# Optimization experiments

Measured on AMD Instinct MI355X. Metric: run time of the kernel, lower is better.

Reference implementation:

```python
import jax, jax.numpy as jnp
import numpy as np

N_NODES = 100000
N_EDGES = 1600000
F_IN = 128
HID = 128
N_LAYERS = 4
N_CLASSES = 10
N_GRAPHS = 512
BN_EPS = 1e-5


def setup_inputs() -> dict:
    key = jax.random.key(0)
    ks = jax.random.split(key, 16)
    x = jax.random.normal(ks[0], (N_NODES, F_IN), dtype=jnp.float32)
    edge_index = jax.random.randint(ks[1], (2, N_EDGES), 0, N_NODES, dtype=jnp.int64)
    edge_attr = jax.random.normal(ks[2], (N_EDGES, 8), dtype=jnp.float32)
    batch = jnp.sort(jax.random.randint(ks[3], (N_NODES,), 0, N_GRAPHS, dtype=jnp.int64))
    # Per-layer MLP params (in-dim is 128 for all layers since F_IN == HID).
    s1 = 1.0 / np.sqrt(F_IN)
    s2 = 1.0 / np.sqrt(2 * HID)
    W1 = jax.random.uniform(ks[4], (N_LAYERS, F_IN, 2 * HID), minval=-s1, maxval=s1, dtype=jnp.float32)
    b1 = jax.random.uniform(ks[5], (N_LAYERS, 2 * HID), minval=-s1, maxval=s1, dtype=jnp.float32)
    gamma1 = jnp.ones((N_LAYERS, 2 * HID), dtype=jnp.float32)
    beta1 = jnp.zeros((N_LAYERS, 2 * HID), dtype=jnp.float32)
    W2 = jax.random.uniform(ks[6], (N_LAYERS, 2 * HID, HID), minval=-s2, maxval=s2, dtype=jnp.float32)
    b2 = jax.random.uniform(ks[7], (N_LAYERS, HID), minval=-s2, maxval=s2, dtype=jnp.float32)
    sf = 1.0 / np.sqrt(HID * N_LAYERS)
    fcW = jax.random.uniform(ks[8], (HID * N_LAYERS, N_CLASSES), minval=-sf, maxval=sf, dtype=jnp.float32)
    fcb = jax.random.uniform(ks[9], (N_CLASSES,), minval=-sf, maxval=sf, dtype=jnp.float32)
    return {"x": x, "edge_index": edge_index, "edge_attr": edge_attr, "batch": batch,
            "W1": W1, "b1": b1, "gamma1": gamma1, "beta1": beta1,
            "W2": W2, "b2": b2, "fcW": fcW, "fcb": fcb}


def reference(x, edge_index, edge_attr, batch, W1, b1, gamma1, beta1, W2, b2, fcW, fcb):
    # edge_attr is unused by the original forward.
    src, dst = edge_index[0], edge_index[1]
    n = x.shape[0]
    # In-degree for mean aggregation (messages flow src -> dst in PyG).
    deg = jax.ops.segment_sum(jnp.ones((src.shape[0],), x.dtype), dst, num_segments=n)
    inv_deg = 1.0 / jnp.maximum(deg, 1.0)
    h = x
    xs = []
    for i in range(N_LAYERS):
        # GINConv, eps=0, aggr='mean': nn(x + mean_j h_j)
        agg = jax.ops.segment_sum(h[src], dst, num_segments=n) * inv_deg[:, None]
        z = h + agg
        z = z @ W1[i] + b1[i]                      # [N, 2H]
        mu = jnp.mean(z, axis=0)
        var = jnp.mean(jnp.square(z - mu), axis=0)  # biased var (BN training mode)
        z = gamma1[i] * (z - mu) * jax.lax.rsqrt(var + BN_EPS) + beta1[i]
        z = jax.nn.relu(z)
        z = z @ W2[i] + b2[i]                      # [N, H]
        h = jax.nn.relu(z)
        xs.append(h)
    xcat = jnp.concatenate(xs, axis=1)             # [N, H*L]
    # global_mean_pool over graph ids
    gsum = jax.ops.segment_sum(xcat, batch, num_segments=N_GRAPHS)
    gcnt = jax.ops.segment_sum(jnp.ones((n,), xcat.dtype), batch, num_segments=N_GRAPHS)
    pooled = gsum / jnp.maximum(gcnt, 1.0)[:, None]
    logits = pooled @ fcW + fcb
    return jax.nn.log_softmax(logits, axis=-1)
```

## Files before the change

kernel.cpp:

```cpp
#include <hip/hip_runtime.h>
#include <cstdint>
#include <cstddef>

#define NN 100000
#define NE 1600000
#define FD 128
#define HD2 256
#define NLAYERS 4
#define NGR 512
#define NCLS 10
#define BNEPS 1e-5f
#define G1TILES 1563
#define GEMM_GRID 521
#define MLP_GRID 256
#define EB 6250
#define NB 391
#define NSLICE 8
#define SLICEW 12500

typedef unsigned short ushort_t;
typedef short bf16x8 __attribute__((ext_vector_type(8)));
typedef float f32x4 __attribute__((ext_vector_type(4)));

__device__ __forceinline__ float bfl(unsigned short u) {
  unsigned v = ((unsigned)u) << 16;
  return __builtin_bit_cast(float, v);
}
__device__ __forceinline__ unsigned short fbf(float f) {
  unsigned u = __builtin_bit_cast(unsigned, f);
  unsigned r = (u + 0x7FFFu + ((u >> 16) & 1u)) >> 16;
  return (unsigned short)r;
}

__global__ void k_init_detect(const int* ei, int* flag, int* degi) {
  int i = blockIdx.x * 256 + threadIdx.x;
  if (i < NN) degi[i] = 0;
  if (blockIdx.x == 0) {
    __shared__ int nz;
    if (threadIdx.x == 0) nz = 0;
    __syncthreads();
    if (ei[2 * threadIdx.x + 1] != 0) atomicAdd(&nz, 1);
    __syncthreads();
    if (threadIdx.x == 0) flag[0] = (nz == 0) ? 1 : 0;
  }
}

__global__ void k_repack(const int* ei, const int* batch, const int* flag,
                         int* src32, int* dst32, int* batch32) {
  int i = blockIdx.x * 256 + threadIdx.x;
  const bool wide = (flag[0] != 0);
  if (i < NE) {
    src32[i] = wide ? ei[2 * i] : ei[i];
    dst32[i] = wide ? ei[2 * (NE + i)] : ei[NE + i];
  }
  if (i < NN) batch32[i] = wide ? batch[2 * i] : batch[i];
}

__global__ void k_deg8(const int* __restrict__ dst, int* degi) {
  int slice = blockIdx.x & (NSLICE - 1);
  int e = (blockIdx.x >> 3) * 256 + threadIdx.x;
  if (e >= NE) return;
  int d = dst[e];
  int lo = slice * SLICEW;
  if (d >= lo && d < lo + SLICEW) atomicAdd(&degi[d], 1);
}

__global__ void k_scan1(const int* degi, int* rowptr, int* bsum) {
  __shared__ int s[256];
  int t = threadIdx.x;
  int i = blockIdx.x * 256 + t;
  int v = (i < NN) ? degi[i] : 0;
  s[t] = v;
  __syncthreads();
  for (int off = 1; off < 256; off <<= 1) {
    int x = (t >= off) ? s[t - off] : 0;
    __syncthreads();
    s[t] += x;
    __syncthreads();
  }
  if (i < NN) rowptr[i] = s[t] - v;
  if (t == 255) bsum[blockIdx.x] = s[255];
}

__global__ void k_scan2_gstats(int* bsum, int nb, const int* __restrict__ batch,
                               int* __restrict__ gstart, int* __restrict__ gcnti) {
  __shared__ int s[512];
  int t = threadIdx.x;
  int v = (t < nb) ? bsum[t] : 0;
  s[t] = v;
  __syncthreads();
  for (int off = 1; off < 512; off <<= 1) {
    int x = (t >= off) ? s[t - off] : 0;
    __syncthreads();
    s[t] += x;
    __syncthreads();
  }
  if (t < nb) bsum[t] = s[t] - v;
  if (t < NGR) {
    int g = t;
    int lo = 0, hi = NN;
    while (lo < hi) { int m = (lo + hi) >> 1; if (batch[m] < g) lo = m + 1; else hi = m; }
    int st = lo;
    hi = NN;
    while (lo < hi) { int m = (lo + hi) >> 1; if (batch[m] < g + 1) lo = m + 1; else hi = m; }
    gstart[g] = st;
    gcnti[g] = lo - st;
  }
}

__global__ void k_scan3_cursor(int* rowptr, const int* bsum, int* cursor,
                               const int* degi, float* inv_deg) {
  int i = blockIdx.x * 256 + threadIdx.x;
  if (i < NN) {
    int r = rowptr[i] + bsum[blockIdx.x];
    rowptr[i] = r;
    cursor[i] = r;
    inv_deg[i] = 1.f / fmaxf((float)degi[i], 1.f);
  }
  if (i == 0) rowptr[NN] = NE;
}

__global__ void k_scatter8(const int* __restrict__ src, const int* __restrict__ dst,
                           int* cursor, int* csr) {
  int slice = blockIdx.x & (NSLICE - 1);
  int e = (blockIdx.x >> 3) * 256 + threadIdx.x;
  if (e >= NE) return;
  int d = dst[e];
  int lo = slice * SLICEW;
  if (d >= lo && d < lo + SLICEW) {
    int p = atomicAdd(&cursor[d], 1);
    csr[p] = src[e];
  }
}

__global__ void k_cvt_x(const float* __restrict__ x, ushort_t* __restrict__ xb) {
  int i = blockIdx.x * 256 + threadIdx.x;
  if (i >= NN * FD / 8) return;
  const float4* p = (const float4*)x + (size_t)i * 2;
  float4 a = p[0], b = p[1];
  bf16x8 o;
  o[0] = (short)fbf(a.x); o[1] = (short)fbf(a.y);
  o[2] = (short)fbf(a.z); o[3] = (short)fbf(a.w);
  o[4] = (short)fbf(b.x); o[5] = (short)fbf(b.y);
  o[6] = (short)fbf(b.z); o[7] = (short)fbf(b.w);
  *(bf16x8*)&xb[(size_t)i * 8] = o;
}

__global__ void k_cvt_w(const float* __restrict__ W1, const float* __restrict__ W2,
                        ushort_t* __restrict__ W1t, ushort_t* __restrict__ W2t) {
  int idx = blockIdx.x * 256 + threadIdx.x;
  if (idx >= NLAYERS * FD * HD2) return;
  int l = idx >> 15, r = idx & 32767;
  {
    int n = r >> 7, k = r & 127;
    W1t[(size_t)l * 32768 + n * 128 + k] = fbf(W1[(size_t)l * 32768 + k * 256 + n]);
  }
  {
    int n = r >> 8, k = r & 255;
    W2t[(size_t)l * 32768 + n * 256 + k] = fbf(W2[(size_t)l * 32768 + k * 128 + n]);
  }
}

__global__ void k_agg(const ushort_t* __restrict__ h, const int* __restrict__ rowptr,
                      const int* __restrict__ csr, const float* __restrict__ inv_deg,
                      ushort_t* __restrict__ tout, float* bnsum) {
  if (blockIdx.x == 0) {
    bnsum[threadIdx.x] = 0.f;
    bnsum[HD2 + threadIdx.x] = 0.f;
  }
  const int wave = threadIdx.x >> 6;
  const int lane = threadIdx.x & 63;
  const int q = lane >> 4, sub = lane & 15;
  const int node = blockIdx.x * 16 + wave * 4 + q;
  const uint4* h16 = (const uint4*)h;
  int beg = rowptr[node];
  int deg = rowptr[node + 1] - beg;
  int m1 = max(deg, __shfl_xor(deg, 16));
  int maxd = max(m1, __shfl_xor(m1, 32));
  float a0 = 0.f, a1 = 0.f, a2 = 0.f, a3 = 0.f;
  float a4 = 0.f, a5 = 0.f, a6 = 0.f, a7 = 0.f;
  int j = 0;
  for (; j + 8 <= maxd; j += 8) {
    uint4 p[8];
#pragma unroll
    for (int u = 0; u < 8; ++u) {
      bool valid = (j + u) < deg;
      int idx = beg + (valid ? j + u : 0);
      int s = csr[idx];
      uint4 v = h16[(size_t)s * 16 + sub];
      p[u].x = valid ? v.x : 0u;
      p[u].y = valid ? v.y : 0u;
      p[u].z = valid ? v.z : 0u;
      p[u].w = valid ? v.w : 0u;
    }
#pragma unroll
    for (int u = 0; u < 8; ++u) {
      a0 += bfl((unsigned short)(p[u].x & 0xFFFF));
      a1 += bfl((unsigned short)(p[u].x >> 16));
      a2 += bfl((unsigned short)(p[u].y & 0xFFFF));
      a3 += bfl((unsigned short)(p[u].y >> 16));
      a4 += bfl((unsigned short)(p[u].z & 0xFFFF));
      a5 += bfl((unsigned short)(p[u].z >> 16));
      a6 += bfl((unsigned short)(p[u].w & 0xFFFF));
      a7 += bfl((unsigned short)(p[u].w >> 16));
    }
  }
  for (; j < maxd; ++j) {
    bool valid = j < deg;
    int idx = beg + (valid ? j : 0);
    int s = csr[idx];
    uint4 v = h16[(size_t)s * 16 + sub];
    if (valid) {
      a0 += bfl((unsigned short)(v.x & 0xFFFF));
      a1 += bfl((unsigned short)(v.x >> 16));
      a2 += bfl((unsigned short)(v.y & 0xFFFF));
      a3 += bfl((unsigned short)(v.y >> 16));
      a4 += bfl((unsigned short)(v.z & 0xFFFF));
      a5 += bfl((unsigned short)(v.z >> 16));
      a6 += bfl((unsigned short)(v.w & 0xFFFF));
      a7 += bfl((unsigned short)(v.w >> 16));
    }
  }
  float id = inv_deg[node];
  uint4 c = h16[(size_t)node * 16 + sub];
  float o0 = bfl((unsigned short)(c.x & 0xFFFF)) + a0 * id;
  float o1 = bfl((unsigned short)(c.x >> 16)) + a1 * id;
  float o2 = bfl((unsigned short)(c.y & 0xFFFF)) + a2 * id;
  float o3 = bfl((unsigned short)(c.y >> 16)) + a3 * id;
  float o4 = bfl((unsigned short)(c.z & 0xFFFF)) + a4 * id;
  float o5 = bfl((unsigned short)(c.z >> 16)) + a5 * id;
  float o6 = bfl((unsigned short)(c.w & 0xFFFF)) + a6 * id;
  float o7 = bfl((unsigned short)(c.w >> 16)) + a7 * id;
  uint4 ow;
  ow.x = (unsigned)fbf(o0) | ((unsigned)fbf(o1) << 16);
  ow.y = (unsigned)fbf(o2) | ((unsigned)fbf(o3) << 16);
  ow.z = (unsigned)fbf(o4) | ((unsigned)fbf(o5) << 16);
  ow.w = (unsigned)fbf(o6) | ((unsigned)fbf(o7) << 16);
  ((uint4*)tout)[(size_t)node * 16 + sub] = ow;
}

__launch_bounds__(256, 2)
__global__ void k_zstat(const ushort_t* __restrict__ A, const ushort_t* __restrict__ Bt,
                        const float* __restrict__ bias, float* __restrict__ bnsum) {
  __shared__ ushort_t Bs[256 * 128];
  __shared__ ushort_t As[64 * 128];
  const int tid = threadIdx.x;
#pragma unroll
  for (int i = 0; i < 16; ++i) {
    int chunk = tid + 256 * i;
    int n = chunk >> 4, c = chunk & 15;
    bf16x8 v = *(const bf16x8*)&Bt[n * 128 + c * 8];
    *(bf16x8*)((char*)Bs + n * 256 + ((c * 16) ^ ((n & 7) << 4))) = v;
  }
  const int wv = tid >> 6, ln = tid & 63;
  const int lr = ln & 15, lg = ln >> 4;
  float bb[16];
#pragma unroll
  for (int nt = 0; nt < 16; ++nt) bb[nt] = bias[nt * 16 + lr];
  float s0[16] = {}, s1[16] = {};

  for (int t = blockIdx.x; t < G1TILES; t += GEMM_GRID) {
    int row0 = t * 64;
#pragma unroll
    for (int i = 0; i < 4; ++i) {
      int chunk = tid + 256 * i;
      int r = chunk >> 4, c = chunk & 15;
      int grow = row0 + r; if (grow >= NN) grow = NN - 1;
      bf16x8 v = *(const bf16x8*)&A[(size_t)grow * FD + c * 8];
      *(bf16x8*)((char*)As + r * 256 + ((c * 16) ^ ((r & 7) << 4))) = v;
    }
    __syncthreads();
    int arow = wv * 16 + lr;
    bf16x8 af[4];
#pragma unroll
    for (int ks = 0; ks < 4; ++ks)
      af[ks] = *(bf16x8*)((char*)As + arow * 256 + ((ks * 64 + lg * 16) ^ ((arow & 7) << 4)));
    f32x4 acc[16];
#pragma unroll
    for (int nt = 0; nt < 16; ++nt) acc[nt] = (f32x4){0.f, 0.f, 0.f, 0.f};
#pragma unroll
    for (int nt = 0; nt < 16; ++nt) {
      int bn = nt * 16 + lr;
#pragma unroll
      for (int ks = 0; ks < 4; ++ks) {
        bf16x8 bfr = *(bf16x8*)((char*)Bs + bn * 256 + ((ks * 64 + lg * 16) ^ ((bn & 7) << 4)));
        acc[nt] = __builtin_amdgcn_mfma_f32_16x16x32_bf16(af[ks], bfr, acc[nt], 0, 0, 0);
      }
    }
    __syncthreads();
#pragma unroll
    for (int nt = 0; nt < 16; ++nt) {
#pragma unroll
      for (int j = 0; j < 4; ++j) {
        int grow = row0 + wv * 16 + lg * 4 + j;
        if (grow < NN) {
          float zf = acc[nt][j] + bb[nt];
          s0[nt] += zf;
          s1[nt] += zf * zf;
        }
      }
    }
  }
  __syncthreads();
  float* ls = (float*)As;
  ls[tid] = 0.f; ls[tid + 256] = 0.f;
  __syncthreads();
#pragma unroll
  for (int nt = 0; nt < 16; ++nt) {
    int col = nt * 16 + lr;
    atomicAdd(&ls[col], s0[nt]);
    atomicAdd(&ls[col + 256], s1[nt]);
  }
  __syncthreads();
  if (tid < 256) {
    atomicAdd(&bnsum[tid], ls[tid]);
    atomicAdd(&bnsum[HD2 + tid], ls[tid + 256]);
  }
}

__launch_bounds__(512, 2)
__global__ void k_mlp(const ushort_t* __restrict__ T, const ushort_t* __restrict__ W1t,
                      const ushort_t* __restrict__ W2t, const float* __restrict__ b1,
                      const float* __restrict__ b2, const float* __restrict__ bnsum,
                      const float* __restrict__ gamma, const float* __restrict__ beta,
                      ushort_t* __restrict__ Hout) {
  __shared__ ushort_t W1s[256 * 128];
  __shared__ ushort_t W2s[128 * 256];
  __shared__ ushort_t ZR[64 * 256];
  const int tid = threadIdx.x;
#pragma unroll
  for (int i = 0; i < 8; ++i) {
    int chunk = tid + 512 * i;
    int n = chunk >> 4, c = chunk & 15;
    bf16x8 v = *(const bf16x8*)&W1t[n * 128 + c * 8];
    *(bf16x8*)((char*)W1s + n * 256 + ((c * 16) ^ ((n & 7) << 4))) = v;
  }
#pragma unroll
  for (int i = 0; i < 8; ++i) {
    int chunk = tid + 512 * i;
    int n = chunk >> 5, c = chunk & 31;
    bf16x8 v = *(const bf16x8*)&W2t[n * 256 + c * 8];
    *(bf16x8*)((char*)W2s + n * 512 + ((c * 16) ^ ((n & 7) << 4))) = v;
  }
  const int wv = tid >> 6, ln = tid & 63;
  const int lr = ln & 15, lg = ln >> 4;
  const int mrow = (wv & 3) * 16;
  const int nh = wv >> 2;
  float a1v[8], a2v[8], bb1[8];
#pragma unroll
  for (int nt = 0; nt < 8; ++nt) {
    int c = (nh * 8 + nt) * 16 + lr;
    float mu = bnsum[c] * (1.f / (float)NN);
    float var = fmaxf(bnsum[HD2 + c] * (1.f / (float)NN) - mu * mu, 0.f);
    float g = gamma[c] * rsqrtf(var + BNEPS);
    a1v[nt] = g;
    a2v[nt] = beta[c] - mu * g;
    bb1[nt] = b1[c];
  }
  float bb2[4];
#pragma unroll
  for (int nt2 = 0; nt2 < 4; ++nt2) bb2[nt2] = b2[nh * 64 + nt2 * 16 + lr];
  __syncthreads();

  for (int t = blockIdx.x; t < G1TILES; t += MLP_GRID) {
    int row0 = t * 64;
    int grow = row0 + mrow + lr; if (grow >= NN) grow = NN - 1;
    bf16x8 af[4];
#pragma unroll
    for (int ks = 0; ks < 4; ++ks)
      af[ks] = *(const bf16x8*)&T[(size_t)grow * FD + ks * 32 + lg * 8];
    f32x4 acc1[8];
#pragma unroll
    for (int nt = 0; nt < 8; ++nt) acc1[nt] = (f32x4){0.f, 0.f, 0.f, 0.f};
#pragma unroll
    for (int nt = 0; nt < 8; ++nt) {
      int bn = (nh * 8 + nt) * 16 + lr;
#pragma unroll
      for (int ks = 0; ks < 4; ++ks) {
        bf16x8 bfr = *(bf16x8*)((char*)W1s + bn * 256 + ((ks * 64 + lg * 16) ^ ((bn & 7) << 4)));
        acc1[nt] = __builtin_amdgcn_mfma_f32_16x16x32_bf16(af[ks], bfr, acc1[nt], 0, 0, 0);
      }
    }
#pragma unroll
    for (int nt = 0; nt < 8; ++nt) {
      int col = (nh * 8 + nt) * 16 + lr;
#pragma unroll
      for (int j = 0; j < 4; ++j) {
        int row = mrow + lg * 4 + j;
        float z = acc1[nt][j] + bb1[nt];
        float f = fmaxf(z * a1v[nt] + a2v[nt], 0.f);
        int byte = row * 512 + ((((col >> 3) << 4) ^ ((row & 7) << 4))) + (col & 7) * 2;
        *(ushort_t*)((char*)ZR + byte) = fbf(f);
      }
    }
    __syncthreads();
    int zrow = mrow + lr;
    bf16x8 af2[8];
#pragma unroll
    for (int ks2 = 0; ks2 < 8; ++ks2) {
      int c2 = ks2 * 4 + lg;
      af2[ks2] = *(bf16x8*)((char*)ZR + zrow * 512 + ((c2 * 16) ^ ((zrow & 7) << 4)));
    }
    __syncthreads();
    f32x4 acc2[4];
#pragma unroll
    for (int nt2 = 0; nt2 < 4; ++nt2) acc2[nt2] = (f32x4){0.f, 0.f, 0.f, 0.f};
#pragma unroll
    for (int nt2 = 0; nt2 < 4; ++nt2) {
      int bn2 = nh * 64 + nt2 * 16 + lr;
#pragma unroll
      for (int ks2 = 0; ks2 < 8; ++ks2) {
        int c2 = ks2 * 4 + lg;
        bf16x8 bfr2 = *(bf16x8*)((char*)W2s + bn2 * 512 + ((c2 * 16) ^ ((bn2 & 7) << 4)));
        acc2[nt2] = __builtin_amdgcn_mfma_f32_16x16x32_bf16(af2[ks2], bfr2, acc2[nt2], 0, 0, 0);
      }
    }
#pragma unroll
    for (int nt2 = 0; nt2 < 4; ++nt2) {
      int col = nh * 64 + nt2 * 16 + lr;
#pragma unroll
      for (int j = 0; j < 4; ++j) {
        int hrow = row0 + mrow + lg * 4 + j;
        if (hrow < NN) Hout[(size_t)hrow * FD + col] = fbf(fmaxf(acc2[nt2][j] + bb2[nt2], 0.f));
      }
    }
  }
}

__launch_bounds__(256)
__global__ void k_pool_fc(const ushort_t* __restrict__ hb, const int* __restrict__ gstart,
                          const int* __restrict__ gcnti, const float* __restrict__ fcW,
                          const float* __restrict__ fcb, float* __restrict__ out) {
  __shared__ float pool4[4][512];
  __shared__ float wred[4][NCLS];
  int g = blockIdx.x, t = threadIdx.x;
  int start = gstart[g], cnt = gcnti[g];
  int chunk = t & 63, ro = t >> 6;
  int L = chunk >> 4, cc = (chunk & 15) * 8;
  const ushort_t* hL = hb + (size_t)L * NN * FD;
  float s[8] = {};
  for (int r = start + ro; r < start + cnt; r += 4) {
    bf16x8 v = *(const bf16x8*)&hL[(size_t)r * FD + cc];
#pragma unroll
    for (int j = 0; j < 8; ++j) s[j] += bfl((unsigned short)v[j]);
  }
#pragma unroll
  for (int j = 0; j < 8; ++j) pool4[ro][chunk * 8 + j] = s[j];
  __syncthreads();
  float inv = 1.f / fmaxf((float)cnt, 1.f);
  float pA = (pool4[0][t] + pool4[1][t] + pool4[2][t] + pool4[3][t]) * inv;
  float pB = (pool4[0][t + 256] + pool4[1][t + 256] + pool4[2][t + 256] + pool4[3][t + 256]) * inv;
  float pacc[NCLS];
#pragma unroll
  for (int c = 0; c < NCLS; ++c)
    pacc[c] = pA * fcW[t * NCLS + c] + pB * fcW[(t + 256) * NCLS + c];
#pragma unroll
  for (int off = 32; off > 0; off >>= 1)
#pragma unroll
    for (int c = 0; c < NCLS; ++c) pacc[c] += __shfl_down(pacc[c], off);
  if ((t & 63) == 0)
#pragma unroll
    for (int c = 0; c < NCLS; ++c) wred[t >> 6][c] = pacc[c];
  __syncthreads();
  if (t == 0) {
    float lg[NCLS];
    float mx = -1e30f;
#pragma unroll
    for (int c = 0; c < NCLS; ++c) {
      lg[c] = wred[0][c] + wred[1][c] + wred[2][c] + wred[3][c] + fcb[c];
      mx = fmaxf(mx, lg[c]);
    }
    float se = 0.f;
#pragma unroll
    for (int c = 0; c < NCLS; ++c) se += expf(lg[c] - mx);
    float lse = mx + logf(se);
#pragma unroll
    for (int c = 0; c < NCLS; ++c) out[(size_t)g * NCLS + c] = lg[c] - lse;
  }
}

extern "C" void kernel_launch(void* const* d_in, const int* in_sizes, int n_in,
                              void* d_out, int out_size, void* d_ws, size_t ws_size,
                              hipStream_t stream) {
  const float* x      = (const float*)d_in[0];
  const int*   ei     = (const int*)d_in[1];
  const int*   batch  = (const int*)d_in[3];
  const float* W1     = (const float*)d_in[4];
  const float* b1     = (const float*)d_in[5];
  const float* gamma1 = (const float*)d_in[6];
  const float* beta1  = (const float*)d_in[7];
  const float* W2     = (const float*)d_in[8];
  const float* b2     = (const float*)d_in[9];
  const float* fcW    = (const float*)d_in[10];
  const float* fcb    = (const float*)d_in[11];
  float* out = (float*)d_out;

  char* p = (char*)d_ws;
  auto alloc = [&](size_t bytes) {
    char* r = p;
    p += (bytes + 255) & ~(size_t)255;
    return r;
  };
  ushort_t* xbf   = (ushort_t*)alloc((size_t)NN * FD * 2);
  ushort_t* tbuf  = (ushort_t*)alloc((size_t)NN * FD * 2);
  ushort_t* hb    = (ushort_t*)alloc((size_t)NLAYERS * NN * FD * 2);
  ushort_t* W1t   = (ushort_t*)alloc((size_t)NLAYERS * FD * HD2 * 2);
  ushort_t* W2t   = (ushort_t*)alloc((size_t)NLAYERS * FD * HD2 * 2);
  float* inv_deg  = (float*)alloc((size_t)NN * 4);
  float* bnsum    = (float*)alloc(2 * HD2 * 4);
  int* degi       = (int*)alloc((size_t)NN * 4);
  int* rowptr     = (int*)alloc((size_t)(NN + 1) * 4);
  int* cursor     = (int*)alloc((size_t)NN * 4);
  int* csr        = (int*)alloc((size_t)NE * 4);
  int* bsum       = (int*)alloc(512 * 4);
  int* src32      = (int*)alloc((size_t)NE * 4);
  int* dst32      = (int*)alloc((size_t)NE * 4);
  int* batch32    = (int*)alloc((size_t)NN * 4);
  int* gcnti      = (int*)alloc((size_t)NGR * 4);
  int* gstart     = (int*)alloc((size_t)NGR * 4);
  int* flag       = (int*)alloc(256);

  k_init_detect<<<NB, 256, 0, stream>>>(ei, flag, degi);
  k_repack<<<EB, 256, 0, stream>>>(ei, batch, flag, src32, dst32, batch32);
  k_deg8<<<EB * NSLICE, 256, 0, stream>>>(dst32, degi);
  k_scan1<<<NB, 256, 0, stream>>>(degi, rowptr, bsum);
  k_scan2_gstats<<<1, 512, 0, stream>>>(bsum, NB, batch32, gstart, gcnti);
  k_scan3_cursor<<<NB, 256, 0, stream>>>(rowptr, bsum, cursor, degi, inv_deg);
  k_scatter8<<<EB * NSLICE, 256, 0, stream>>>(src32, dst32, cursor, csr);
  k_cvt_x<<<(NN * FD / 8 + 255) / 256, 256, 0, stream>>>(x, xbf);
  k_cvt_w<<<(NLAYERS * FD * HD2 + 255) / 256, 256, 0, stream>>>(W1, W2, W1t, W2t);

  const ushort_t* hin = xbf;
  for (int L = 0; L < NLAYERS; ++L) {
    k_agg<<<NN / 16, 256, 0, stream>>>(hin, rowptr, csr, inv_deg, tbuf, bnsum);
    k_zstat<<<GEMM_GRID, 256, 0, stream>>>(tbuf, W1t + (size_t)L * FD * HD2,
                                           b1 + (size_t)L * HD2, bnsum);
    k_mlp<<<MLP_GRID, 512, 0, stream>>>(tbuf, W1t + (size_t)L * FD * HD2,
                                        W2t + (size_t)L * FD * HD2,
                                        b1 + (size_t)L * HD2, b2 + (size_t)L * FD,
                                        bnsum, gamma1 + (size_t)L * HD2,
                                        beta1 + (size_t)L * HD2,
                                        hb + (size_t)L * NN * FD);
    hin = hb + (size_t)L * NN * FD;
  }
  k_pool_fc<<<NGR, 256, 0, stream>>>(hb, gstart, gcnti, fcW, fcb, out);
}
```

Baseline: 794.8 us.

## Compute batchnorm statistics from input Gram matrix instead of full first GEMM

Measured after the change: 851.9 us. +7.2%, slower.

```diff
diff --git a/kernel.cpp b/kernel.cpp
--- a/kernel.cpp
+++ b/kernel.cpp
@@ -11,8 +11,8 @@
 #define NCLS 10
 #define BNEPS 1e-5f
 #define G1TILES 1563
-#define GEMM_GRID 521
 #define MLP_GRID 256
+#define GRAM_GRID 256
 #define EB 6250
 #define NB 391
 #define NSLICE 8
@@ -163,11 +163,8 @@
 
 __global__ void k_agg(const ushort_t* __restrict__ h, const int* __restrict__ rowptr,
                       const int* __restrict__ csr, const float* __restrict__ inv_deg,
-                      ushort_t* __restrict__ tout, float* bnsum) {
-  if (blockIdx.x == 0) {
-    bnsum[threadIdx.x] = 0.f;
-    bnsum[HD2 + threadIdx.x] = 0.f;
-  }
+                      ushort_t* __restrict__ tout, float* sbuf) {
+  if (blockIdx.x == 0 && threadIdx.x < FD) sbuf[threadIdx.x] = 0.f;
   const int wave = threadIdx.x >> 6;
   const int lane = threadIdx.x & 63;
   const int q = lane >> 4, sub = lane & 15;
@@ -239,82 +236,135 @@
   ((uint4*)tout)[(size_t)node * 16 + sub] = ow;
 }
 
-__launch_bounds__(256, 2)
-__global__ void k_zstat(const ushort_t* __restrict__ A, const ushort_t* __restrict__ Bt,
-                        const float* __restrict__ bias, float* __restrict__ bnsum) {
-  __shared__ ushort_t Bs[256 * 128];
-  __shared__ ushort_t As[64 * 128];
+__launch_bounds__(256)
+__global__ void k_gram(const ushort_t* __restrict__ T, float* __restrict__ Pg,
+                       float* __restrict__ sbuf) {
+  __shared__ ushort_t Tt[128 * 64];
   const int tid = threadIdx.x;
-#pragma unroll
-  for (int i = 0; i < 16; ++i) {
-    int chunk = tid + 256 * i;
-    int n = chunk >> 4, c = chunk & 15;
-    bf16x8 v = *(const bf16x8*)&Bt[n * 128 + c * 8];
-    *(bf16x8*)((char*)Bs + n * 256 + ((c * 16) ^ ((n & 7) << 4))) = v;
-  }
   const int wv = tid >> 6, ln = tid & 63;
   const int lr = ln & 15, lg = ln >> 4;
-  float bb[16];
-#pragma unroll
-  for (int nt = 0; nt < 16; ++nt) bb[nt] = bias[nt * 16 + lr];
-  float s0[16] = {}, s1[16] = {};
-
-  for (int t = blockIdx.x; t < G1TILES; t += GEMM_GRID) {
+  const int mbase = (wv >> 1) * 64, nbase = (wv & 1) * 64;
+  const int cst = tid & 15;
+  float sloc[8] = {};
+  f32x4 acc[4][4];
+#pragma unroll
+  for (int a = 0; a < 4; ++a)
+#pragma unroll
+    for (int b = 0; b < 4; ++b) acc[a][b] = (f32x4){0.f, 0.f, 0.f, 0.f};
+
+  for (int t = blockIdx.x; t < G1TILES; t += GRAM_GRID) {
     int row0 = t * 64;
 #pragma unroll
     for (int i = 0; i < 4; ++i) {
       int chunk = tid + 256 * i;
-      int r = chunk >> 4, c = chunk & 15;
-      int grow = row0 + r; if (grow >= NN) grow = NN - 1;
-      bf16x8 v = *(const bf16x8*)&A[(size_t)grow * FD + c * 8];
-      *(bf16x8*)((char*)As + r * 256 + ((c * 16) ^ ((r & 7) << 4))) = v;
-    }
-    __syncthreads();
-    int arow = wv * 16 + lr;
-    bf16x8 af[4];
-#pragma unroll
-    for (int ks = 0; ks < 4; ++ks)
-      af[ks] = *(bf16x8*)((char*)As + arow * 256 + ((ks * 64 + lg * 16) ^ ((arow & 7) << 4)));
-    f32x4 acc[16];
-#pragma unroll
-    for (int nt = 0; nt < 16; ++nt) acc[nt] = (f32x4){0.f, 0.f, 0.f, 0.f};
-#pragma unroll
-    for (int nt = 0; nt < 16; ++nt) {
-      int bn = nt * 16 + lr;
-#pragma unroll
-      for (int ks = 0; ks < 4; ++ks) {
-        bf16x8 bfr = *(bf16x8*)((char*)Bs + bn * 256 + ((ks * 64 + lg * 16) ^ ((bn & 7) << 4)));
-        acc[nt] = __builtin_amdgcn_mfma_f32_16x16x32_bf16(af[ks], bfr, acc[nt], 0, 0, 0);
-      }
-    }
-    __syncthreads();
-#pragma unroll
-    for (int nt = 0; nt < 16; ++nt) {
+      int r = chunk >> 4;
+      int grow = row0 + r;
+      uint4 v = (grow < NN) ? ((const uint4*)T)[(size_t)grow * 16 + cst]
+                            : make_uint4(0u, 0u, 0u, 0u);
+      unsigned short us[8];
+      us[0] = (unsigned short)(v.x & 0xFFFF); us[1] = (unsigned short)(v.x >> 16);
+      us[2] = (unsigned short)(v.y & 0xFFFF); us[3] = (unsigned short)(v.y >> 16);
+      us[4] = (unsigned short)(v.z & 0xFFFF); us[5] = (unsigned short)(v.z >> 16);
+      us[6] = (unsigned short)(v.w & 0xFFFF); us[7] = (unsigned short)(v.w >> 16);
+#pragma unroll
+      for (int jj = 0; jj < 8; ++jj) {
+        int j = (jj + (tid & 7)) & 7;
+        int f = cst * 8 + j;
+        int byte = f * 128 + ((((r >> 3) << 4) ^ ((f & 7) << 4))) + (r & 7) * 2;
+        *(ushort_t*)((char*)Tt + byte) = us[j];
+      }
+#pragma unroll
+      for (int j = 0; j < 8; ++j) sloc[j] += bfl(us[j]);
+    }
+    __syncthreads();
+#pragma unroll
+    for (int ks = 0; ks < 2; ++ks) {
+      bf16x8 bfr[4];
+#pragma unroll
+      for (int b = 0; b < 4; ++b) {
+        int fB = nbase + b * 16 + lr;
+        bfr[b] = *(bf16x8*)((char*)Tt + fB * 128 + ((((ks * 4 + lg) << 4) ^ ((fB & 7) << 4))));
+      }
+#pragma unroll
+      for (int a = 0; a < 4; ++a) {
+        int fA = mbase + a * 16 + lr;
+        bf16x8 afr = *(bf16x8*)((char*)Tt + fA * 128 + ((((ks * 4 + lg) << 4) ^ ((fA & 7) << 4))));
+#pragma unroll
+        for (int b = 0; b < 4; ++b)
+          acc[a][b] = __builtin_amdgcn_mfma_f32_16x16x32_bf16(afr, bfr[b], acc[a][b], 0, 0, 0);
+      }
+    }
+    __syncthreads();
+  }
+  float* sred = (float*)Tt;
+#pragma unroll
+  for (int j = 0; j < 8; ++j) sred[(tid >> 4) * 128 + cst * 8 + j] = sloc[j];
+  __syncthreads();
+  if (tid < FD) {
+    float v = 0.f;
+#pragma unroll
+    for (int g = 0; g < 16; ++g) v += sred[g * 128 + tid];
+    atomicAdd(&sbuf[tid], v);
+  }
+  float* P = Pg + (size_t)blockIdx.x * (FD * FD);
+#pragma unroll
+  for (int a = 0; a < 4; ++a)
+#pragma unroll
+    for (int b = 0; b < 4; ++b)
 #pragma unroll
       for (int j = 0; j < 4; ++j) {
-        int grow = row0 + wv * 16 + lg * 4 + j;
-        if (grow < NN) {
-          float zf = acc[nt][j] + bb[nt];
-          s0[nt] += zf;
-          s1[nt] += zf * zf;
-        }
-      }
-    }
-  }
-  __syncthreads();
-  float* ls = (float*)As;
-  ls[tid] = 0.f; ls[tid + 256] = 0.f;
-  __syncthreads();
-#pragma unroll
-  for (int nt = 0; nt < 16; ++nt) {
-    int col = nt * 16 + lr;
-    atomicAdd(&ls[col], s0[nt]);
-    atomicAdd(&ls[col + 256], s1[nt]);
-  }
-  __syncthreads();
-  if (tid < 256) {
-    atomicAdd(&bnsum[tid], ls[tid]);
-    atomicAdd(&bnsum[HD2 + tid], ls[tid + 256]);
+        int fm = mbase + a * 16 + (ln >> 4) * 4 + j;
+        int fn = nbase + b * 16 + lr;
+        P[fm * FD + fn] = acc[a][b][j];
+      }
+}
+
+__global__ void k_gred(const float* __restrict__ Pg, float* __restrict__ G) {
+  int idx = blockIdx.x * 256 + threadIdx.x;
+  float v = 0.f;
+  for (int b = 0; b < GRAM_GRID; ++b) v += Pg[(size_t)b * (FD * FD) + idx];
+  G[idx] = v;
+}
+
+__launch_bounds__(256)
+__global__ void k_bnfin2(const float* __restrict__ G, const float* __restrict__ sbuf,
+                         const float* __restrict__ W1, const float* __restrict__ b1,
+                         float* __restrict__ bnsum) {
+  __shared__ float Gs[FD * FD];
+  __shared__ float ws1[FD * 32];
+  const int tid = threadIdx.x;
+  for (int i = tid; i < FD * FD; i += 256) Gs[i] = G[i];
+  for (int i = tid; i < FD * 32; i += 256) {
+    int k = i >> 5, cl = i & 31;
+    ws1[i] = bfl(fbf(W1[k * HD2 + blockIdx.x * 32 + cl]));
+  }
+  __syncthreads();
+  const int cl = tid & 31, kg = tid >> 5;
+  float q = 0.f, sd = 0.f;
+  for (int k = kg * 16; k < kg * 16 + 16; ++k) {
+    float wk = ws1[k * 32 + cl];
+    float dot = 0.f;
+#pragma unroll 8
+    for (int k2 = 0; k2 < FD; ++k2) dot += Gs[k * FD + k2] * ws1[k2 * 32 + cl];
+    q += wk * dot;
+    sd += sbuf[k] * wk;
+  }
+  __syncthreads();
+  float* red = Gs;
+  red[tid] = q;
+  red[256 + tid] = sd;
+  __syncthreads();
+  if (tid < 32) {
+    float Q = 0.f, SD = 0.f;
+#pragma unroll
+    for (int g = 0; g < 8; ++g) {
+      Q += red[tid + 32 * g];
+      SD += red[256 + tid + 32 * g];
+    }
+    int c = blockIdx.x * 32 + tid;
+    float bb = b1[c];
+    bnsum[c] = SD + (float)NN * bb;
+    bnsum[HD2 + c] = Q + 2.f * bb * SD + (float)NN * bb * bb;
   }
 }
 
@@ -508,6 +558,9 @@
   ushort_t* W2t   = (ushort_t*)alloc((size_t)NLAYERS * FD * HD2 * 2);
   float* inv_deg  = (float*)alloc((size_t)NN * 4);
   float* bnsum    = (float*)alloc(2 * HD2 * 4);
+  float* Pg       = (float*)alloc((size_t)GRAM_GRID * FD * FD * 4);
+  float* Gm       = (float*)alloc((size_t)FD * FD * 4);
+  float* sbuf     = (float*)alloc((size_t)FD * 4);
   int* degi       = (int*)alloc((size_t)NN * 4);
   int* rowptr     = (int*)alloc((size_t)(NN + 1) * 4);
   int* cursor     = (int*)alloc((size_t)NN * 4);
@@ -532,9 +585,11 @@
 
   const ushort_t* hin = xbf;
   for (int L = 0; L < NLAYERS; ++L) {
-    k_agg<<<NN / 16, 256, 0, stream>>>(hin, rowptr, csr, inv_deg, tbuf, bnsum);
-    k_zstat<<<GEMM_GRID, 256, 0, stream>>>(tbuf, W1t + (size_t)L * FD * HD2,
-                                           b1 + (size_t)L * HD2, bnsum);
+    k_agg<<<NN / 16, 256, 0, stream>>>(hin, rowptr, csr, inv_deg, tbuf, sbuf);
+    k_gram<<<GRAM_GRID, 256, 0, stream>>>(tbuf, Pg, sbuf);
+    k_gred<<<64, 256, 0, stream>>>(Pg, Gm);
+    k_bnfin2<<<8, 256, 0, stream>>>(Gm, sbuf, W1 + (size_t)L * FD * HD2,
+                                    b1 + (size_t)L * HD2, bnsum);
     k_mlp<<<MLP_GRID, 512, 0, stream>>>(tbuf, W1t + (size_t)L * FD * HD2,
                                         W2t + (size_t)L * FD * HD2,
                                         b1 + (size_t)L * HD2, b2 + (size_t)L * FD,
```
